# Kernel optimization log

Measured on AMD Instinct MI355X. Metric: run time of the kernel, lower is better.

Reference implementation:

```python
import jax, jax.numpy as jnp
import numpy as np

R, A, B = 32, 16, 65536  # rules, antecedents, samples


def setup_inputs() -> dict:
    key = jax.random.key(0)
    k1, k2, k3 = jax.random.split(key, 3)
    input_data = jax.random.normal(k1, (B, A), dtype=jnp.float32)
    # abs(normal) like the original init; shift/scale keeps sigmas >= 1 so the
    # product of A Gaussian memberships stays well above fp32 underflow.
    FRB_W = jnp.abs(jax.random.normal(k2, (2 * R * A,), dtype=jnp.float32)) * 0.5 + 1.0
    C = jnp.abs(jax.random.normal(k3, (R, A + 1), dtype=jnp.float32))
    return {"input_data": input_data, "FRB_W": FRB_W, "C": C}


def reference(input_data, FRB_W, C):
    Rn = C.shape[0]
    An = C.shape[1] - 1
    # Faithful to the original indexing: locat_num = A*i + k, Gauss1 mf uses
    # FRB_weights[locat_num : locat_num+2] = (sigma, center) (overlapping windows).
    idx = jnp.arange(Rn)[:, None] * An + jnp.arange(An)[None, :]  # [R, A]
    sigma = FRB_W[idx]          # [R, A]
    center = FRB_W[idx + 1]     # [R, A]
    # Gauss1mf(x, [sigma, c]) = exp(-0.5 * ((x - c) / sigma)^2)
    z = (input_data[:, None, :] - center[None]) / sigma[None]      # [B, R, A]
    u = jnp.exp(-0.5 * z * z)                                      # [B, R, A]
    UU = jnp.prod(u, axis=-1)                                      # [B, R] rule firing strengths
    # TSK first-order consequent: C[:,0] bias + C[:,1:] @ x
    C_help = input_data @ C[:, 1:].T + C[:, 0]                     # [B, R]
    # weighted average over rules
    return jnp.sum(UU * C_help, axis=-1) / jnp.sum(UU, axis=-1)    # [B]
```

## Files before the change

kernel.cpp:

```cpp
#include <hip/hip_runtime.h>

#define RR 32
#define AA 16
#define BLOCK 256


__global__ __launch_bounds__(512) void tsk_precompute(
    const float* __restrict__ W,
    const float* __restrict__ C,
    float* __restrict__ P)
{
    __shared__ float cpart[RR * AA];
    const float LOG2E = 1.4426950408889634f;
    int t = threadIdx.x;
    if (t < RR * AA) {
        int r = t >> 4, k = t & 15;
        float sig = W[t];
        float c   = W[t + 1];
        float inv2 = 1.0f / (sig * sig);
        P[r * 64 + k]      = -0.5f * inv2 * LOG2E;
        P[r * 64 + 16 + k] = c * inv2 * LOG2E;
        cpart[t]           = -0.5f * c * c * inv2 * LOG2E;
        P[r * 64 + 32 + k] = C[r * (AA + 1) + 1 + k];
    }
    __syncthreads();
    if (t < RR) {
        float s = 0.0f;
        #pragma unroll
        for (int k = 0; k < AA; ++k) s += cpart[t * AA + k];
        P[t * 64 + 49] = s;
        P[t * 64 + 48] = C[t * (AA + 1)];
    }
}

__global__ __launch_bounds__(BLOCK, 1) void tsk_main(
    const float* __restrict__ x,
    const float* __restrict__ P,
    float* __restrict__ out,
    int B)
{
    int b = blockIdx.x * BLOCK + threadIdx.x;
    if (b >= B) return;

    const float4* xr = (const float4*)(x + (size_t)b * AA);
    float4 v0 = xr[0], v1 = xr[1], v2 = xr[2], v3 = xr[3];
    float xv[AA] = { v0.x, v0.y, v0.z, v0.w,
                     v1.x, v1.y, v1.z, v1.w,
                     v2.x, v2.y, v2.z, v2.w,
                     v3.x, v3.y, v3.z, v3.w };
    float x2[AA];
    #pragma unroll
    for (int k = 0; k < AA; ++k) x2[k] = xv[k] * xv[k];

    float num = 0.0f, den = 0.0f;
    #pragma unroll 2
    for (int r = 0; r < RR; ++r) {
        const float* p = P + r * 64;
        float ea = 0.0f, eb = 0.0f;
        float ch = p[48];
        #pragma unroll
        for (int k = 0; k < AA; ++k) {
            ea = fmaf(p[k],      x2[k], ea);
            eb = fmaf(p[16 + k], xv[k], eb);
            ch = fmaf(p[32 + k], xv[k], ch);
        }
        float w = exp2f(ea + eb + p[49]);
        num = fmaf(w, ch, num);
        den += w;
    }
    out[b] = num / den;
}

extern "C" void kernel_launch(void* const* d_in, const int* in_sizes, int n_in,
                              void* d_out, int out_size, void* d_ws, size_t ws_size,
                              hipStream_t stream) {
    const float* x = (const float*)d_in[0];
    const float* W = (const float*)d_in[1];
    const float* C = (const float*)d_in[2];
    float* out = (float*)d_out;
    float* P = (float*)d_ws;
    int B = in_sizes[0] / AA;

    tsk_precompute<<<dim3(1), dim3(512), 0, stream>>>(W, C, P);
    tsk_main<<<dim3((B + BLOCK - 1) / BLOCK), dim3(BLOCK), 0, stream>>>(x, P, out, B);
}
```

Baseline: 74.57 us.

## Split rules across four waves per sample block and reduce via shared memory

Each block now handles 64 samples, and its four waves each evaluate one quarter of the 32 rules. Partial numerators and denominators are combined through shared memory. This quadruples the grid, from 256 blocks to 1024, so the GPU's many CUs get more waves and latency hiding improves. The change also swaps in raw hardware exp2 and reciprocal intrinsics and raises the launch-bounds occupancy hint. In exchange it adds a barrier, redundant x loads per wave, and slightly lower precision from the approximate reciprocal.

```diff
diff --git a/kernel.cpp b/kernel.cpp
--- a/kernel.cpp
+++ b/kernel.cpp
@@ -2,7 +2,10 @@
 
 #define RR 32
 #define AA 16
+#define SPLIT 4
+#define RPW (RR / SPLIT)
 #define BLOCK 256
+#define SPB 64
 
 
 __global__ __launch_bounds__(512) void tsk_precompute(
@@ -33,16 +36,22 @@
     }
 }
 
-__global__ __launch_bounds__(BLOCK, 1) void tsk_main(
+__global__ __launch_bounds__(BLOCK, 4) void tsk_main(
     const float* __restrict__ x,
     const float* __restrict__ P,
     float* __restrict__ out,
     int B)
 {
-    int b = blockIdx.x * BLOCK + threadIdx.x;
-    if (b >= B) return;
+    __shared__ float pnum[SPLIT][SPB];
+    __shared__ float pden[SPLIT][SPB];
 
-    const float4* xr = (const float4*)(x + (size_t)b * AA);
+    const int lane = threadIdx.x & 63;
+    const int wv = __builtin_amdgcn_readfirstlane(threadIdx.x >> 6);
+
+    int s = blockIdx.x * SPB + lane;
+    int sl = s < B ? s : B - 1;
+
+    const float4* xr = (const float4*)(x + (size_t)sl * AA);
     float4 v0 = xr[0], v1 = xr[1], v2 = xr[2], v3 = xr[3];
     float xv[AA] = { v0.x, v0.y, v0.z, v0.w,
                      v1.x, v1.y, v1.z, v1.w,
@@ -53,9 +62,10 @@
     for (int k = 0; k < AA; ++k) x2[k] = xv[k] * xv[k];
 
     float num = 0.0f, den = 0.0f;
+    const float* pw = P + wv * RPW * 64;
     #pragma unroll 2
-    for (int r = 0; r < RR; ++r) {
-        const float* p = P + r * 64;
+    for (int r = 0; r < RPW; ++r) {
+        const float* p = pw + r * 64;
         float ea = 0.0f, eb = 0.0f;
         float ch = p[48];
         #pragma unroll
@@ -64,11 +74,22 @@
             eb = fmaf(p[16 + k], xv[k], eb);
             ch = fmaf(p[32 + k], xv[k], ch);
         }
-        float w = exp2f(ea + eb + p[49]);
+        float w = __builtin_amdgcn_exp2f(ea + eb + p[49]);
         num = fmaf(w, ch, num);
         den += w;
     }
-    out[b] = num / den;
+
+    pnum[wv][lane] = num;
+    pden[wv][lane] = den;
+    __syncthreads();
+
+    if (threadIdx.x < SPB) {
+        int t = threadIdx.x;
+        float n = pnum[0][t] + pnum[1][t] + pnum[2][t] + pnum[3][t];
+        float d = pden[0][t] + pden[1][t] + pden[2][t] + pden[3][t];
+        int so = blockIdx.x * SPB + t;
+        if (so < B) out[so] = n * __builtin_amdgcn_rcpf(d);
+    }
 }
 
 extern "C" void kernel_launch(void* const* d_in, const int* in_sizes, int n_in,
@@ -82,5 +103,5 @@
     int B = in_sizes[0] / AA;
 
     tsk_precompute<<<dim3(1), dim3(512), 0, stream>>>(W, C, P);
-    tsk_main<<<dim3((B + BLOCK - 1) / BLOCK), dim3(BLOCK), 0, stream>>>(x, P, out, B);
+    tsk_main<<<dim3((B + SPB - 1) / SPB), dim3(BLOCK), 0, stream>>>(x, P, out, B);
 }
```

After: 63.35 us. 1.18x faster.
